# Performance work log

Hardware: AMD Instinct MI355X
Metric: run time of the kernel (lower is better)

The kernel has to match this reference:

```python
import jax, jax.numpy as jnp
import numpy as np

N_NODES = 100000
N_EDGES = 1600000
IN_C = 64
HID_C = 64
OUT_C = 8


def _glorot(key, shape):
    fan_in, fan_out = shape
    lim = (6.0 / (fan_in + fan_out)) ** 0.5
    return jax.random.uniform(key, shape, jnp.float32, -lim, lim)


def setup_inputs() -> dict:
    key = jax.random.key(0)
    ks = jax.random.split(key, 16)
    inp = {
        "x": jax.random.normal(ks[0], (N_NODES, IN_C), jnp.float32),
        "edge_index": jax.random.randint(ks[1], (2, N_EDGES), 0, N_NODES, jnp.int64),
        "edge_attr": jax.random.normal(ks[2], (N_EDGES, 1), jnp.float32),
        # GIN MLP params: layer i uses Linear(in,h) -> ReLU -> Linear(h,h)
        "l0_w1": _glorot(ks[3], (IN_C, HID_C)), "l0_b1": jnp.zeros((HID_C,), jnp.float32),
        "l0_w2": _glorot(ks[4], (HID_C, HID_C)), "l0_b2": jnp.zeros((HID_C,), jnp.float32),
        "l1_w1": _glorot(ks[5], (HID_C, HID_C)), "l1_b1": jnp.zeros((HID_C,), jnp.float32),
        "l1_w2": _glorot(ks[6], (HID_C, HID_C)), "l1_b2": jnp.zeros((HID_C,), jnp.float32),
        # last layer maps hidden -> out (reduce_dims is None)
        "l2_w1": _glorot(ks[7], (HID_C, OUT_C)), "l2_b1": jnp.zeros((OUT_C,), jnp.float32),
        "l2_w2": _glorot(ks[8], (OUT_C, OUT_C)), "l2_b2": jnp.zeros((OUT_C,), jnp.float32),
    }
    return inp


def _gin_layer(x, src, dst, w1, b1, w2, b2):
    # GINConv with eps=0: out_i = MLP(x_i + sum_{j->i} x_j)
    agg = jax.ops.segment_sum(x[src], dst, num_segments=N_NODES)  # [N, C]
    h = x + agg
    h = jax.nn.relu(h @ w1 + b1)
    return h @ w2 + b2


def reference(x, edge_index, edge_attr,
              l0_w1, l0_b1, l0_w2, l0_b2,
              l1_w1, l1_b1, l1_w2, l1_b2,
              l2_w1, l2_b1, l2_w2, l2_b2):
    src, dst = edge_index[0], edge_index[1]
    # dropout is identity in eval mode
    h = _gin_layer(x, src, dst, l0_w1, l0_b1, l0_w2, l0_b2)
    h = jax.nn.relu(h)
    h = _gin_layer(h, src, dst, l1_w1, l1_b1, l1_w2, l1_b2)
    h = jax.nn.relu(h)
    h = _gin_layer(h, src, dst, l2_w1, l2_b1, l2_w2, l2_b2)  # no relu on last (reduce_dims None)
    return jax.nn.log_softmax(h, axis=-1)
```

## Files before the change

kernel.cpp:

```cpp
#include <hip/hip_runtime.h>
#include <math.h>

#define N_NODES 100000
#define N_EDGES 1600000
#define C 64
#define OUTC 8
#define NBUCK 256
#define BRANGE 391
#define BCAP 7200
#define CNT_PAD 64
#define BUCK_CHUNK 4096
#define SGRP 25
#define HSZ (BRANGE * SGRP)

__device__ __forceinline__ float bflo(unsigned u) { return __uint_as_float(u << 16); }
__device__ __forceinline__ float bfhi(unsigned u) { return __uint_as_float(u & 0xFFFF0000u); }
__device__ __forceinline__ unsigned short f2bf(float f) {
    unsigned b = __float_as_uint(f);
    b += 0x7FFFu + ((b >> 16) & 1u);
    return (unsigned short)(b >> 16);
}

__global__ __launch_bounds__(256) void bucket_k(const int* __restrict__ src, const int* __restrict__ dst,
                                                int* cntp, uint2* __restrict__ ebuf, int ne) {
    __shared__ int lcnt[NBUCK], lbase[NBUCK], lcur[NBUCK];
    int t = threadIdx.x;
    if (t < NBUCK) { lcnt[t] = 0; lcur[t] = 0; }
    __syncthreads();
    int base = blockIdx.x * BUCK_CHUNK;
#pragma unroll
    for (int i = 0; i < BUCK_CHUNK / 256; i++) {
        int e = base + i * 256 + t;
        if (e < ne) {
            int d = __builtin_nontemporal_load(dst + e);
            atomicAdd(&lcnt[d / BRANGE], 1);
        }
    }
    __syncthreads();
    if (t < NBUCK) lbase[t] = lcnt[t] ? atomicAdd(&cntp[t * CNT_PAD], lcnt[t]) : 0;
    __syncthreads();
#pragma unroll
    for (int i = 0; i < BUCK_CHUNK / 256; i++) {
        int e = base + i * 256 + t;
        if (e < ne) {
            int d = __builtin_nontemporal_load(dst + e);
            int s = __builtin_nontemporal_load(src + e);
            int r = d / BRANGE;
            int pos = lbase[r] + atomicAdd(&lcur[r], 1);
            if (pos < BCAP) ebuf[(size_t)r * BCAP + pos] = make_uint2((unsigned)s, (unsigned)d);
        }
    }
}

__global__ __launch_bounds__(512) void fill5_k(const int* __restrict__ cntp, const uint2* __restrict__ ebuf,
                                               int* __restrict__ rowptr, int* __restrict__ ssrc) {
    __shared__ int H[HSZ];
    __shared__ int part[512];
    __shared__ int cbuf[NBUCK];
    __shared__ int bbase;
    int b = blockIdx.x;
    int lo = b * BRANGE;
    int span = N_NODES - lo; if (span > BRANGE) span = BRANGE; if (span < 0) span = 0;
    int t = threadIdx.x;
    for (int i = t; i < HSZ; i += 512) H[i] = 0;
    if (t < NBUCK) cbuf[t] = cntp[t * CNT_PAD];
    __syncthreads();
    if (t == 0) {
        int s = 0;
        for (int i = 0; i < b; i++) s += cbuf[i];
        bbase = s;
    }
    int cnt = cbuf[b];
    if (cnt > BCAP) cnt = BCAP;
    const uint2* buf = ebuf + (size_t)b * BCAP;
    for (int i = t; i < cnt; i += 512) {
        uint2 ed = buf[i];
        atomicAdd(&H[((int)ed.y - lo) * SGRP + ((int)ed.x >> 12)], 1);
    }
    __syncthreads();
    const int IPT = 20;
    int base = t * IPT, s = 0;
#pragma unroll
    for (int i = 0; i < IPT; i++) { int idx = base + i; if (idx < HSZ) s += H[idx]; }
    part[t] = s;
    __syncthreads();
    for (int off = 1; off < 512; off <<= 1) {
        int u = (t >= off) ? part[t - off] : 0;
        __syncthreads();
        part[t] += u;
        __syncthreads();
    }
    int run = part[t] - s;
#pragma unroll
    for (int i = 0; i < IPT; i++) {
        int idx = base + i;
        if (idx < HSZ) { int v = H[idx]; H[idx] = run; run += v; }
    }
    __syncthreads();
    if (t < span) rowptr[lo + t] = bbase + H[t * SGRP];
    if (b == NBUCK - 1 && t == 0) rowptr[N_NODES] = N_EDGES;
    __syncthreads();
    for (int i = t; i < cnt; i += 512) {
        uint2 ed = buf[i];
        int p = bbase + atomicAdd(&H[((int)ed.y - lo) * SGRP + ((int)ed.x >> 12)], 1);
        ssrc[p] = (int)ed.x;
    }
}

__global__ __launch_bounds__(256) void conv_bf16_k(const float* __restrict__ in, unsigned short* __restrict__ outb, int nElem) {
    int i = blockIdx.x * 256 + threadIdx.x;
    int stride = gridDim.x * 256;
    for (int e = i * 4; e < nElem; e += stride * 4) {
        float4 v = *(const float4*)(in + e);
        ushort4 o;
        o.x = f2bf(v.x); o.y = f2bf(v.y); o.z = f2bf(v.z); o.w = f2bf(v.w);
        *(ushort4*)(outb + e) = o;
    }
}

__global__ __launch_bounds__(256) void gather_bf16_k(const unsigned short* __restrict__ featb,
                                                     const int* __restrict__ rowptr,
                                                     const int* __restrict__ ssrc,
                                                     float* __restrict__ tout, int n) {
    const uint2* feat2 = (const uint2*)featb;
    int lane = threadIdx.x & 63;
    int slot = lane >> 4;
    int chg  = lane & 15;
    int wid = blockIdx.x * 4 + (threadIdx.x >> 6);
    if (wid >= n) return;
    int beg = rowptr[wid], end = rowptr[wid + 1];
    float ax = 0.f, ay = 0.f, az = 0.f, aw = 0.f;
    if (slot == 0) {
        uint2 v = feat2[(size_t)wid * 16 + chg];
        ax = bflo(v.x); ay = bfhi(v.x); az = bflo(v.y); aw = bfhi(v.y);
    }
    int e = beg;
    for (; e + 16 <= end; e += 16) {
        int i0 = ssrc[e + slot];
        int i1 = ssrc[e + 4 + slot];
        int i2 = ssrc[e + 8 + slot];
        int i3 = ssrc[e + 12 + slot];
        uint2 v0 = feat2[(size_t)i0 * 16 + chg];
        uint2 v1 = feat2[(size_t)i1 * 16 + chg];
        uint2 v2 = feat2[(size_t)i2 * 16 + chg];
        uint2 v3 = feat2[(size_t)i3 * 16 + chg];
        ax += (bflo(v0.x) + bflo(v1.x)) + (bflo(v2.x) + bflo(v3.x));
        ay += (bfhi(v0.x) + bfhi(v1.x)) + (bfhi(v2.x) + bfhi(v3.x));
        az += (bflo(v0.y) + bflo(v1.y)) + (bflo(v2.y) + bflo(v3.y));
        aw += (bfhi(v0.y) + bfhi(v1.y)) + (bfhi(v2.y) + bfhi(v3.y));
    }
    for (; e + 4 <= end; e += 4) {
        int i = ssrc[e + slot];
        uint2 v = feat2[(size_t)i * 16 + chg];
        ax += bflo(v.x); ay += bfhi(v.x); az += bflo(v.y); aw += bfhi(v.y);
    }
    if (e + slot < end) {
        int i = ssrc[e + slot];
        uint2 v = feat2[(size_t)i * 16 + chg];
        ax += bflo(v.x); ay += bfhi(v.x); az += bflo(v.y); aw += bfhi(v.y);
    }
    ax += __shfl_xor(ax, 16, 64); ay += __shfl_xor(ay, 16, 64);
    az += __shfl_xor(az, 16, 64); aw += __shfl_xor(aw, 16, 64);
    ax += __shfl_xor(ax, 32, 64); ay += __shfl_xor(ay, 32, 64);
    az += __shfl_xor(az, 32, 64); aw += __shfl_xor(aw, 32, 64);
    if (slot == 0) ((float4*)tout)[(size_t)wid * 16 + chg] = make_float4(ax, ay, az, aw);
}

__global__ __launch_bounds__(256) void fused_final_bf16_k(const unsigned short* __restrict__ featb,
                                                          const int* __restrict__ rowptr,
                                                          const int* __restrict__ ssrc,
                                                          float* __restrict__ out,
                                                          const float* __restrict__ W1, const float* __restrict__ b1,
                                                          const float* __restrict__ W2, const float* __restrict__ b2,
                                                          int n) {
    const uint2* feat2 = (const uint2*)featb;
    int lane = threadIdx.x & 63;
    int slot = lane >> 4;
    int chg  = lane & 15;
    int j = lane & 7;
    int g = lane >> 3;
    float w1r[8], w2r[8];
#pragma unroll
    for (int i = 0; i < 8; i++) w1r[i] = W1[(g * 8 + i) * OUTC + j];
#pragma unroll
    for (int i = 0; i < 8; i++) w2r[i] = W2[i * OUTC + j];
    float b1j = b1[j], b2j = b2[j];
    int wid = blockIdx.x * 4 + (threadIdx.x >> 6);
    if (wid >= n) return;
    int beg = rowptr[wid], end = rowptr[wid + 1];
    float ax = 0.f, ay = 0.f, az = 0.f, aw = 0.f;
    if (slot == 0) {
        uint2 v = feat2[(size_t)wid * 16 + chg];
        ax = bflo(v.x); ay = bfhi(v.x); az = bflo(v.y); aw = bfhi(v.y);
    }
    int e = beg;
    for (; e + 16 <= end; e += 16) {
        int i0 = ssrc[e + slot];
        int i1 = ssrc[e + 4 + slot];
        int i2 = ssrc[e + 8 + slot];
        int i3 = ssrc[e + 12 + slot];
        uint2 v0 = feat2[(size_t)i0 * 16 + chg];
        uint2 v1 = feat2[(size_t)i1 * 16 + chg];
        uint2 v2 = feat2[(size_t)i2 * 16 + chg];
        uint2 v3 = feat2[(size_t)i3 * 16 + chg];
        ax += (bflo(v0.x) + bflo(v1.x)) + (bflo(v2.x) + bflo(v3.x));
        ay += (bfhi(v0.x) + bfhi(v1.x)) + (bfhi(v2.x) + bfhi(v3.x));
        az += (bflo(v0.y) + bflo(v1.y)) + (bflo(v2.y) + bflo(v3.y));
        aw += (bfhi(v0.y) + bfhi(v1.y)) + (bfhi(v2.y) + bfhi(v3.y));
    }
    for (; e + 4 <= end; e += 4) {
        int i = ssrc[e + slot];
        uint2 v = feat2[(size_t)i * 16 + chg];
        ax += bflo(v.x); ay += bfhi(v.x); az += bflo(v.y); aw += bfhi(v.y);
    }
    if (e + slot < end) {
        int i = ssrc[e + slot];
        uint2 v = feat2[(size_t)i * 16 + chg];
        ax += bflo(v.x); ay += bfhi(v.x); az += bflo(v.y); aw += bfhi(v.y);
    }
    ax += __shfl_xor(ax, 16, 64); ay += __shfl_xor(ay, 16, 64);
    az += __shfl_xor(az, 16, 64); aw += __shfl_xor(aw, 16, 64);
    ax += __shfl_xor(ax, 32, 64); ay += __shfl_xor(ay, 32, 64);
    az += __shfl_xor(az, 32, 64); aw += __shfl_xor(aw, 32, 64);
    float h = 0.f;
#pragma unroll
    for (int i = 0; i < 8; i++) {
        float compv = (i & 3) == 0 ? ax : (i & 3) == 1 ? ay : (i & 3) == 2 ? az : aw;
        float tm = __shfl(compv, g * 2 + (i >> 2), 64);
        h = fmaf(tm, w1r[i], h);
    }
    h += __shfl_xor(h, 8, 64);
    h += __shfl_xor(h, 16, 64);
    h += __shfl_xor(h, 32, 64);
    h = fmaxf(h + b1j, 0.f);
    float y = b2j;
#pragma unroll
    for (int k = 0; k < 8; k++) {
        float hk = __shfl(h, (lane & ~7) + k, 64);
        y = fmaf(hk, w2r[k], y);
    }
    float m = y;
    m = fmaxf(m, __shfl_xor(m, 1, 64));
    m = fmaxf(m, __shfl_xor(m, 2, 64));
    m = fmaxf(m, __shfl_xor(m, 4, 64));
    float ex = expf(y - m);
    float ssum = ex;
    ssum += __shfl_xor(ssum, 1, 64);
    ssum += __shfl_xor(ssum, 2, 64);
    ssum += __shfl_xor(ssum, 4, 64);
    float res = (y - m) - logf(ssum);
    if (lane < 8) out[(size_t)wid * OUTC + lane] = res;
}

__global__ __launch_bounds__(256) void mlp_gemm_k(const float* __restrict__ tin,
                                                  unsigned short* __restrict__ zoutb,
                                                  const float* __restrict__ W1, const float* __restrict__ b1,
                                                  const float* __restrict__ W2, const float* __restrict__ b2,
                                                  int relu_out) {
    __shared__ float Tl[64][64];
    __shared__ float W1l[64][64];
    __shared__ float W2l[64][64];
    int t = threadIdx.x;
    int nbase = blockIdx.x * 64;
    {
        const float4* w1v = (const float4*)W1; const float4* w2v = (const float4*)W2;
        float4* w1d = (float4*)&W1l[0][0];     float4* w2d = (float4*)&W2l[0][0];
#pragma unroll
        for (int i = 0; i < 4; i++) { w1d[t + 256 * i] = w1v[t + 256 * i]; w2d[t + 256 * i] = w2v[t + 256 * i]; }
    }
    {
        int n = t >> 2, c0 = (t & 3) * 16;
        int gn = nbase + n;
        float4 r[4];
        if (gn < N_NODES) {
#pragma unroll
            for (int i = 0; i < 4; i++) r[i] = *(const float4*)&tin[(size_t)gn * 64 + c0 + 4 * i];
        } else {
#pragma unroll
            for (int i = 0; i < 4; i++) r[i] = make_float4(0.f, 0.f, 0.f, 0.f);
        }
#pragma unroll
        for (int i = 0; i < 4; i++) {
            Tl[c0 + 4 * i + 0][n] = r[i].x; Tl[c0 + 4 * i + 1][n] = r[i].y;
            Tl[c0 + 4 * i + 2][n] = r[i].z; Tl[c0 + 4 * i + 3][n] = r[i].w;
        }
    }
    __syncthreads();
    int tn = t & 15, tc = t >> 4;
    float b1v[4], b2v[4];
#pragma unroll
    for (int i = 0; i < 4; i++) { b1v[i] = b1[4 * tc + i]; b2v[i] = b2[4 * tc + i]; }
    float acc[4][4];
#pragma unroll
    for (int i = 0; i < 4; i++)
#pragma unroll
        for (int j = 0; j < 4; j++) acc[i][j] = 0.f;
#pragma unroll 8
    for (int k = 0; k < 64; k++) {
        float4 tv = *(const float4*)&Tl[k][4 * tn];
        float4 wv = *(const float4*)&W1l[k][4 * tc];
        acc[0][0] = fmaf(wv.x, tv.x, acc[0][0]); acc[0][1] = fmaf(wv.x, tv.y, acc[0][1]);
        acc[0][2] = fmaf(wv.x, tv.z, acc[0][2]); acc[0][3] = fmaf(wv.x, tv.w, acc[0][3]);
        acc[1][0] = fmaf(wv.y, tv.x, acc[1][0]); acc[1][1] = fmaf(wv.y, tv.y, acc[1][1]);
        acc[1][2] = fmaf(wv.y, tv.z, acc[1][2]); acc[1][3] = fmaf(wv.y, tv.w, acc[1][3]);
        acc[2][0] = fmaf(wv.z, tv.x, acc[2][0]); acc[2][1] = fmaf(wv.z, tv.y, acc[2][1]);
        acc[2][2] = fmaf(wv.z, tv.z, acc[2][2]); acc[2][3] = fmaf(wv.z, tv.w, acc[2][3]);
        acc[3][0] = fmaf(wv.w, tv.x, acc[3][0]); acc[3][1] = fmaf(wv.w, tv.y, acc[3][1]);
        acc[3][2] = fmaf(wv.w, tv.z, acc[3][2]); acc[3][3] = fmaf(wv.w, tv.w, acc[3][3]);
    }
    __syncthreads();
#pragma unroll
    for (int i = 0; i < 4; i++) {
        float4 hv;
        hv.x = fmaxf(acc[i][0] + b1v[i], 0.f); hv.y = fmaxf(acc[i][1] + b1v[i], 0.f);
        hv.z = fmaxf(acc[i][2] + b1v[i], 0.f); hv.w = fmaxf(acc[i][3] + b1v[i], 0.f);
        *(float4*)&Tl[4 * tc + i][4 * tn] = hv;
    }
#pragma unroll
    for (int i = 0; i < 4; i++)
#pragma unroll
        for (int j = 0; j < 4; j++) acc[i][j] = 0.f;
    __syncthreads();
#pragma unroll 8
    for (int k = 0; k < 64; k++) {
        float4 tv = *(const float4*)&Tl[k][4 * tn];
        float4 wv = *(const float4*)&W2l[k][4 * tc];
        acc[0][0] = fmaf(wv.x, tv.x, acc[0][0]); acc[0][1] = fmaf(wv.x, tv.y, acc[0][1]);
        acc[0][2] = fmaf(wv.x, tv.z, acc[0][2]); acc[0][3] = fmaf(wv.x, tv.w, acc[0][3]);
        acc[1][0] = fmaf(wv.y, tv.x, acc[1][0]); acc[1][1] = fmaf(wv.y, tv.y, acc[1][1]);
        acc[1][2] = fmaf(wv.y, tv.z, acc[1][2]); acc[1][3] = fmaf(wv.y, tv.w, acc[1][3]);
        acc[2][0] = fmaf(wv.z, tv.x, acc[2][0]); acc[2][1] = fmaf(wv.z, tv.y, acc[2][1]);
        acc[2][2] = fmaf(wv.z, tv.z, acc[2][2]); acc[2][3] = fmaf(wv.z, tv.w, acc[2][3]);
        acc[3][0] = fmaf(wv.w, tv.x, acc[3][0]); acc[3][1] = fmaf(wv.w, tv.y, acc[3][1]);
        acc[3][2] = fmaf(wv.w, tv.z, acc[3][2]); acc[3][3] = fmaf(wv.w, tv.w, acc[3][3]);
    }
    unsigned short* ob = (unsigned short*)&W1l[0][0];
#pragma unroll
    for (int j = 0; j < 4; j++) {
        float y0 = acc[0][j] + b2v[0], y1 = acc[1][j] + b2v[1];
        float y2 = acc[2][j] + b2v[2], y3 = acc[3][j] + b2v[3];
        if (relu_out) {
            y0 = fmaxf(y0, 0.f); y1 = fmaxf(y1, 0.f);
            y2 = fmaxf(y2, 0.f); y3 = fmaxf(y3, 0.f);
        }
        uint2 p;
        p.x = (unsigned)f2bf(y0) | ((unsigned)f2bf(y1) << 16);
        p.y = (unsigned)f2bf(y2) | ((unsigned)f2bf(y3) << 16);
        *(uint2*)&ob[(4 * tn + j) * 64 + 4 * tc] = p;
    }
    __syncthreads();
    {
        const uint4* sb = (const uint4*)ob;
        uint4* gb = (uint4*)(zoutb + (size_t)nbase * 64);
        size_t elemBase = (size_t)nbase * 64;
#pragma unroll
        for (int s = 0; s < 2; s++) {
            int idx = 2 * t + s;
            if (elemBase + (size_t)idx * 8 < (size_t)N_NODES * 64) gb[idx] = sb[idx];
        }
    }
}

extern "C" void kernel_launch(void* const* d_in, const int* in_sizes, int n_in,
                              void* d_out, int out_size, void* d_ws, size_t ws_size,
                              hipStream_t stream) {
    const float* x = (const float*)d_in[0];
    const int* ei = (const int*)d_in[1];
    const float* l0w1 = (const float*)d_in[3],  *l0b1 = (const float*)d_in[4];
    const float* l0w2 = (const float*)d_in[5],  *l0b2 = (const float*)d_in[6];
    const float* l1w1 = (const float*)d_in[7],  *l1b1 = (const float*)d_in[8];
    const float* l1w2 = (const float*)d_in[9],  *l1b2 = (const float*)d_in[10];
    const float* l2w1 = (const float*)d_in[11], *l2b1 = (const float*)d_in[12];
    const float* l2w2 = (const float*)d_in[13], *l2b2 = (const float*)d_in[14];
    float* out = (float*)d_out;
    const int* src = ei;
    const int* dst = ei + N_EDGES;

    char* ws = (char*)d_ws;
    size_t off = 0;
    auto carve = [&](size_t bytes) -> void* {
        void* p = ws + off;
        off += (bytes + 255) & ~(size_t)255;
        return p;
    };
    int* cntp   = (int*)carve((size_t)NBUCK * CNT_PAD * 4);
    int* rowptr = (int*)carve((size_t)(N_NODES + 1) * 4);
    int* ssrc   = (int*)carve((size_t)N_EDGES * 4);
    unsigned short* xb = (unsigned short*)carve((size_t)N_NODES * C * 2);
    unsigned short* zb = (unsigned short*)carve((size_t)(N_NODES + 64) * C * 2);
    float* tb   = (float*)carve((size_t)N_NODES * C * 4);
    uint2* ebuf = (uint2*)tb;
    (void)ws_size;

    (void)hipMemsetAsync(cntp, 0, (size_t)NBUCK * CNT_PAD * 4, stream);
    bucket_k<<<(N_EDGES + BUCK_CHUNK - 1) / BUCK_CHUNK, 256, 0, stream>>>(src, dst, cntp, ebuf, N_EDGES);
    fill5_k<<<NBUCK, 512, 0, stream>>>(cntp, ebuf, rowptr, ssrc);

    conv_bf16_k<<<2048, 256, 0, stream>>>(x, xb, N_NODES * C);

    int gblocks = (N_NODES + 3) / 4;
    int mblocks = (N_NODES + 63) / 64;
    gather_bf16_k<<<gblocks, 256, 0, stream>>>(xb, rowptr, ssrc, tb, N_NODES);
    mlp_gemm_k<<<mblocks, 256, 0, stream>>>(tb, zb, l0w1, l0b1, l0w2, l0b2, 1);
    gather_bf16_k<<<gblocks, 256, 0, stream>>>(zb, rowptr, ssrc, tb, N_NODES);
    mlp_gemm_k<<<mblocks, 256, 0, stream>>>(tb, zb, l1w1, l1b1, l1w2, l1b2, 1);
    fused_final_bf16_k<<<gblocks, 256, 0, stream>>>(zb, rowptr, ssrc, out, l2w1, l2b1, l2w2, l2b2, N_NODES);
}
```

Baseline: 276.2 us.

## Store aggregates as bf16, stage edges in LDS, drop source-subgroup CSR sort

```diff
diff --git a/kernel.cpp b/kernel.cpp
--- a/kernel.cpp
+++ b/kernel.cpp
@@ -10,8 +10,6 @@
 #define BCAP 7200
 #define CNT_PAD 64
 #define BUCK_CHUNK 4096
-#define SGRP 25
-#define HSZ (BRANGE * SGRP)
 
 __device__ __forceinline__ float bflo(unsigned u) { return __uint_as_float(u << 16); }
 __device__ __forceinline__ float bfhi(unsigned u) { return __uint_as_float(u & 0xFFFF0000u); }
@@ -20,10 +18,14 @@
     b += 0x7FFFu + ((b >> 16) & 1u);
     return (unsigned short)(b >> 16);
 }
+__device__ __forceinline__ unsigned pk2(float lo, float hi) {
+    return (unsigned)f2bf(lo) | ((unsigned)f2bf(hi) << 16);
+}
 
 __global__ __launch_bounds__(256) void bucket_k(const int* __restrict__ src, const int* __restrict__ dst,
                                                 int* cntp, uint2* __restrict__ ebuf, int ne) {
     __shared__ int lcnt[NBUCK], lbase[NBUCK], lcur[NBUCK];
+    __shared__ uint2 estage[BUCK_CHUNK];
     int t = threadIdx.x;
     if (t < NBUCK) { lcnt[t] = 0; lcur[t] = 0; }
     __syncthreads();
@@ -31,38 +33,41 @@
 #pragma unroll
     for (int i = 0; i < BUCK_CHUNK / 256; i++) {
         int e = base + i * 256 + t;
+        uint2 ed = make_uint2(0xFFFFFFFFu, 0xFFFFFFFFu);
         if (e < ne) {
+            int s = __builtin_nontemporal_load(src + e);
             int d = __builtin_nontemporal_load(dst + e);
+            ed = make_uint2((unsigned)s, (unsigned)d);
             atomicAdd(&lcnt[d / BRANGE], 1);
         }
+        estage[i * 256 + t] = ed;
     }
     __syncthreads();
     if (t < NBUCK) lbase[t] = lcnt[t] ? atomicAdd(&cntp[t * CNT_PAD], lcnt[t]) : 0;
     __syncthreads();
 #pragma unroll
     for (int i = 0; i < BUCK_CHUNK / 256; i++) {
-        int e = base + i * 256 + t;
-        if (e < ne) {
-            int d = __builtin_nontemporal_load(dst + e);
-            int s = __builtin_nontemporal_load(src + e);
-            int r = d / BRANGE;
+        uint2 ed = estage[i * 256 + t];
+        if (ed.y != 0xFFFFFFFFu) {
+            int r = (int)ed.y / BRANGE;
             int pos = lbase[r] + atomicAdd(&lcur[r], 1);
-            if (pos < BCAP) ebuf[(size_t)r * BCAP + pos] = make_uint2((unsigned)s, (unsigned)d);
+            if (pos < BCAP) ebuf[(size_t)r * BCAP + pos] = ed;
         }
     }
 }
 
-__global__ __launch_bounds__(512) void fill5_k(const int* __restrict__ cntp, const uint2* __restrict__ ebuf,
+__global__ __launch_bounds__(512) void fill4_k(const int* __restrict__ cntp, const uint2* __restrict__ ebuf,
                                                int* __restrict__ rowptr, int* __restrict__ ssrc) {
-    __shared__ int H[HSZ];
-    __shared__ int part[512];
+    __shared__ int lcnt[BRANGE];
+    __shared__ int sm[512];
+    __shared__ int lcur[BRANGE];
     __shared__ int cbuf[NBUCK];
     __shared__ int bbase;
     int b = blockIdx.x;
     int lo = b * BRANGE;
     int span = N_NODES - lo; if (span > BRANGE) span = BRANGE; if (span < 0) span = 0;
     int t = threadIdx.x;
-    for (int i = t; i < HSZ; i += 512) H[i] = 0;
+    if (t < BRANGE) lcnt[t] = 0;
     if (t < NBUCK) cbuf[t] = cntp[t * CNT_PAD];
     __syncthreads();
     if (t == 0) {
@@ -75,34 +80,25 @@
     const uint2* buf = ebuf + (size_t)b * BCAP;
     for (int i = t; i < cnt; i += 512) {
         uint2 ed = buf[i];
-        atomicAdd(&H[((int)ed.y - lo) * SGRP + ((int)ed.x >> 12)], 1);
-    }
-    __syncthreads();
-    const int IPT = 20;
-    int base = t * IPT, s = 0;
-#pragma unroll
-    for (int i = 0; i < IPT; i++) { int idx = base + i; if (idx < HSZ) s += H[idx]; }
-    part[t] = s;
+        atomicAdd(&lcnt[(int)ed.y - lo], 1);
+    }
+    __syncthreads();
+    int v = (t < BRANGE) ? lcnt[t] : 0;
+    sm[t] = v;
     __syncthreads();
     for (int off = 1; off < 512; off <<= 1) {
-        int u = (t >= off) ? part[t - off] : 0;
+        int u = (t >= off) ? sm[t - off] : 0;
         __syncthreads();
-        part[t] += u;
+        sm[t] += u;
         __syncthreads();
     }
-    int run = part[t] - s;
-#pragma unroll
-    for (int i = 0; i < IPT; i++) {
-        int idx = base + i;
-        if (idx < HSZ) { int v = H[idx]; H[idx] = run; run += v; }
-    }
-    __syncthreads();
-    if (t < span) rowptr[lo + t] = bbase + H[t * SGRP];
+    int ex = bbase + sm[t] - v;
+    if (t < span) { rowptr[lo + t] = ex; lcur[t] = ex; }
     if (b == NBUCK - 1 && t == 0) rowptr[N_NODES] = N_EDGES;
     __syncthreads();
     for (int i = t; i < cnt; i += 512) {
         uint2 ed = buf[i];
-        int p = bbase + atomicAdd(&H[((int)ed.y - lo) * SGRP + ((int)ed.x >> 12)], 1);
+        int p = atomicAdd(&lcur[(int)ed.y - lo], 1);
         ssrc[p] = (int)ed.x;
     }
 }
@@ -121,7 +117,7 @@
 __global__ __launch_bounds__(256) void gather_bf16_k(const unsigned short* __restrict__ featb,
                                                      const int* __restrict__ rowptr,
                                                      const int* __restrict__ ssrc,
-                                                     float* __restrict__ tout, int n) {
+                                                     unsigned short* __restrict__ toutb, int n) {
     const uint2* feat2 = (const uint2*)featb;
     int lane = threadIdx.x & 63;
     int slot = lane >> 4;
@@ -163,7 +159,12 @@
     az += __shfl_xor(az, 16, 64); aw += __shfl_xor(aw, 16, 64);
     ax += __shfl_xor(ax, 32, 64); ay += __shfl_xor(ay, 32, 64);
     az += __shfl_xor(az, 32, 64); aw += __shfl_xor(aw, 32, 64);
-    if (slot == 0) ((float4*)tout)[(size_t)wid * 16 + chg] = make_float4(ax, ay, az, aw);
+    if (slot == 0) {
+        uint2 o;
+        o.x = pk2(ax, ay);
+        o.y = pk2(az, aw);
+        *(uint2*)&toutb[(size_t)wid * C + chg * 4] = o;
+    }
 }
 
 __global__ __launch_bounds__(256) void fused_final_bf16_k(const unsigned short* __restrict__ featb,
@@ -252,7 +253,7 @@
     if (lane < 8) out[(size_t)wid * OUTC + lane] = res;
 }
 
-__global__ __launch_bounds__(256) void mlp_gemm_k(const float* __restrict__ tin,
+__global__ __launch_bounds__(256) void mlp_gemm_k(const unsigned short* __restrict__ tinb,
                                                   unsigned short* __restrict__ zoutb,
                                                   const float* __restrict__ W1, const float* __restrict__ b1,
                                                   const float* __restrict__ W2, const float* __restrict__ b2,
@@ -271,19 +272,19 @@
     {
         int n = t >> 2, c0 = (t & 3) * 16;
         int gn = nbase + n;
-        float4 r[4];
+        uint4 a = make_uint4(0, 0, 0, 0), b = make_uint4(0, 0, 0, 0);
         if (gn < N_NODES) {
-#pragma unroll
-            for (int i = 0; i < 4; i++) r[i] = *(const float4*)&tin[(size_t)gn * 64 + c0 + 4 * i];
-        } else {
-#pragma unroll
-            for (int i = 0; i < 4; i++) r[i] = make_float4(0.f, 0.f, 0.f, 0.f);
+            const uint4* xr = (const uint4*)&tinb[(size_t)gn * 64 + c0];
+            a = xr[0]; b = xr[1];
         }
-#pragma unroll
-        for (int i = 0; i < 4; i++) {
-            Tl[c0 + 4 * i + 0][n] = r[i].x; Tl[c0 + 4 * i + 1][n] = r[i].y;
-            Tl[c0 + 4 * i + 2][n] = r[i].z; Tl[c0 + 4 * i + 3][n] = r[i].w;
-        }
+        Tl[c0 +  0][n] = bflo(a.x); Tl[c0 +  1][n] = bfhi(a.x);
+        Tl[c0 +  2][n] = bflo(a.y); Tl[c0 +  3][n] = bfhi(a.y);
+        Tl[c0 +  4][n] = bflo(a.z); Tl[c0 +  5][n] = bfhi(a.z);
+        Tl[c0 +  6][n] = bflo(a.w); Tl[c0 +  7][n] = bfhi(a.w);
+        Tl[c0 +  8][n] = bflo(b.x); Tl[c0 +  9][n] = bfhi(b.x);
+        Tl[c0 + 10][n] = bflo(b.y); Tl[c0 + 11][n] = bfhi(b.y);
+        Tl[c0 + 12][n] = bflo(b.z); Tl[c0 + 13][n] = bfhi(b.z);
+        Tl[c0 + 14][n] = bflo(b.w); Tl[c0 + 15][n] = bfhi(b.w);
     }
     __syncthreads();
     int tn = t & 15, tc = t >> 4;
@@ -344,8 +345,8 @@
             y2 = fmaxf(y2, 0.f); y3 = fmaxf(y3, 0.f);
         }
         uint2 p;
-        p.x = (unsigned)f2bf(y0) | ((unsigned)f2bf(y1) << 16);
-        p.y = (unsigned)f2bf(y2) | ((unsigned)f2bf(y3) << 16);
+        p.x = pk2(y0, y1);
+        p.y = pk2(y2, y3);
         *(uint2*)&ob[(4 * tn + j) * 64 + 4 * tc] = p;
     }
     __syncthreads();
@@ -386,23 +387,23 @@
     int* cntp   = (int*)carve((size_t)NBUCK * CNT_PAD * 4);
     int* rowptr = (int*)carve((size_t)(N_NODES + 1) * 4);
     int* ssrc   = (int*)carve((size_t)N_EDGES * 4);
-    unsigned short* xb = (unsigned short*)carve((size_t)N_NODES * C * 2);
-    unsigned short* zb = (unsigned short*)carve((size_t)(N_NODES + 64) * C * 2);
-    float* tb   = (float*)carve((size_t)N_NODES * C * 4);
-    uint2* ebuf = (uint2*)tb;
+    unsigned short* xb  = (unsigned short*)carve((size_t)N_NODES * C * 2);
+    unsigned short* zb  = (unsigned short*)carve((size_t)(N_NODES + 64) * C * 2);
+    unsigned short* tbb = (unsigned short*)carve((size_t)(N_NODES + 64) * C * 2);
+    uint2* ebuf = (uint2*)xb;
     (void)ws_size;
 
     (void)hipMemsetAsync(cntp, 0, (size_t)NBUCK * CNT_PAD * 4, stream);
     bucket_k<<<(N_EDGES + BUCK_CHUNK - 1) / BUCK_CHUNK, 256, 0, stream>>>(src, dst, cntp, ebuf, N_EDGES);
-    fill5_k<<<NBUCK, 512, 0, stream>>>(cntp, ebuf, rowptr, ssrc);
+    fill4_k<<<NBUCK, 512, 0, stream>>>(cntp, ebuf, rowptr, ssrc);
 
     conv_bf16_k<<<2048, 256, 0, stream>>>(x, xb, N_NODES * C);
 
     int gblocks = (N_NODES + 3) / 4;
     int mblocks = (N_NODES + 63) / 64;
-    gather_bf16_k<<<gblocks, 256, 0, stream>>>(xb, rowptr, ssrc, tb, N_NODES);
-    mlp_gemm_k<<<mblocks, 256, 0, stream>>>(tb, zb, l0w1, l0b1, l0w2, l0b2, 1);
-    gather_bf16_k<<<gblocks, 256, 0, stream>>>(zb, rowptr, ssrc, tb, N_NODES);
-    mlp_gemm_k<<<mblocks, 256, 0, stream>>>(tb, zb, l1w1, l1b1, l1w2, l1b2, 1);
+    gather_bf16_k<<<gblocks, 256, 0, stream>>>(xb, rowptr, ssrc, tbb, N_NODES);
+    mlp_gemm_k<<<mblocks, 256, 0, stream>>>(tbb, zb, l0w1, l0b1, l0w2, l0b2, 1);
+    gather_bf16_k<<<gblocks, 256, 0, stream>>>(zb, rowptr, ssrc, tbb, N_NODES);
+    mlp_gemm_k<<<mblocks, 256, 0, stream>>>(tbb, zb, l1w1, l1b1, l1w2, l1b2, 1);
     fused_final_bf16_k<<<gblocks, 256, 0, stream>>>(zb, rowptr, ssrc, out, l2w1, l2b1, l2w2, l2b2, N_NODES);
 }
```

Result: faster. 260.6 us (-5.6%).
